# Performance work log

Measured on AMD Instinct MI355X. Metric: run time of the kernel, lower is better.

Reference implementation:

```python
import jax, jax.numpy as jnp
import numpy as np

DIM = 1024
HEADS = 16
HEAD_DIM = DIM // HEADS


def apply_rope(x):
    # x: (B, S, H, D)
    B, S, H, D = x.shape
    half = D // 2
    freqs = 1.0 / (10000.0 ** (jnp.arange(half, dtype=jnp.float32) / half))
    pos = jnp.arange(S, dtype=jnp.float32)
    angles = pos[:, None] * freqs[None, :]          # (S, half)
    sin = jnp.sin(angles)[None, :, None, :]
    cos = jnp.cos(angles)[None, :, None, :]
    x1, x2 = x[..., :half], x[..., half:]
    return jnp.concatenate([x1 * cos - x2 * sin, x1 * sin + x2 * cos], axis=-1)


def setup_inputs() -> dict:
    key = jax.random.key(0)
    ks = jax.random.split(key, 5)
    x = jax.random.normal(ks[0], (2, 2048, DIM), dtype=jnp.float32)
    s = 1.0 / np.sqrt(DIM)
    qkv_w = jax.random.uniform(ks[1], (3 * DIM, DIM), minval=-s, maxval=s, dtype=jnp.float32)
    qkv_b = jax.random.uniform(ks[2], (3 * DIM,), minval=-s, maxval=s, dtype=jnp.float32)
    proj_w = jax.random.uniform(ks[3], (DIM, DIM), minval=-s, maxval=s, dtype=jnp.float32)
    proj_b = jax.random.uniform(ks[4], (DIM,), minval=-s, maxval=s, dtype=jnp.float32)
    return {"x": x, "qkv_w": qkv_w, "qkv_b": qkv_b, "proj_w": proj_w, "proj_b": proj_b}


def reference(x, qkv_w, qkv_b, proj_w, proj_b):
    B, S, D = x.shape
    qkv = x @ qkv_w.T + qkv_b                       # (B, S, 3D)
    q, k, v = jnp.split(qkv, 3, axis=-1)
    q = q.reshape(B, S, HEADS, HEAD_DIM)
    k = k.reshape(B, S, HEADS, HEAD_DIM)
    v = v.reshape(B, S, HEADS, HEAD_DIM)
    q = apply_rope(q)
    k = apply_rope(k)
    scale = 1.0 / np.sqrt(HEAD_DIM)
    attn = jnp.einsum('bqhd,bkhd->bhqk', q, k) * scale
    mask = jnp.triu(jnp.ones((S, S), dtype=bool), k=1)
    attn = jnp.where(mask[None, None], -1e9, attn)
    attn = jax.nn.softmax(attn, axis=-1)
    out = jnp.einsum('bhqk,bkhd->bqhd', attn, v).reshape(B, S, D)
    return out @ proj_w.T + proj_b
```

## Files before the change

### kernel.cpp

```cpp
#include <hip/hip_runtime.h>
#include <hip/hip_bf16.h>
#include <stdint.h>

typedef unsigned short u16;
typedef __attribute__((ext_vector_type(8))) short bf16x8;
typedef __attribute__((ext_vector_type(4))) float f32x4;
typedef __attribute__((ext_vector_type(16))) float f32x16;

typedef __attribute__((address_space(1))) const void gas_t;
typedef __attribute__((address_space(3))) void las_t;

#define DEV __device__ __forceinline__

DEV float bf2f(u16 v){ union{uint32_t u; float f;} x; x.u = ((uint32_t)v)<<16; return x.f; }
DEV u16 f2bf(float f){ union{float f; uint32_t u;} x; x.f=f; uint32_t r = x.u + 0x7fff + ((x.u>>16)&1u); return (u16)(r>>16); }

DEV uint32_t pk2(float a, float b){
  return (uint32_t)f2bf(a) | ((uint32_t)f2bf(b)<<16);
}

DEV uint32_t cvtpk(float a, float b){
  uint32_t r;
  asm("v_cvt_pk_bf16_f32 %0, %1, %2" : "=v"(r) : "v"(a), "v"(b));
  return r;
}

DEV void xswap(uint32_t a, uint32_t b, int hi, uint32_t& ra, uint32_t& rb){
#if __has_builtin(__builtin_amdgcn_permlane32_swap)
  auto r = __builtin_amdgcn_permlane32_swap((int)a, (int)b, false, false);
  ra = (uint32_t)r[0]; rb = (uint32_t)r[1];
#else
  uint32_t sa = (uint32_t)__shfl_xor((int)a, 32);
  uint32_t sb = (uint32_t)__shfl_xor((int)b, 32);
  ra = hi ? sb : a;
  rb = hi ? b  : sa;
#endif
}

DEV void gload_lds16(const u16* g, u16* l){
  __builtin_amdgcn_global_load_lds((gas_t*)g, (las_t*)l, 16, 0, 0);
}

__global__ void cvt_f32_bf16(const float* __restrict__ src, u16* __restrict__ dst, int n4){
  int i = blockIdx.x*blockDim.x + threadIdx.x;
  if(i < n4){
    float4 v = ((const float4*)src)[i];
    ushort4 o; o.x=f2bf(v.x); o.y=f2bf(v.y); o.z=f2bf(v.z); o.w=f2bf(v.w);
    ((ushort4*)dst)[i] = o;
  }
}

template<int OUT_F32, int SWZ>
__global__ __launch_bounds__(256,3)
void gemm_bt(const u16* __restrict__ A, const u16* __restrict__ Bw,
             const float* __restrict__ bias, void* __restrict__ Cp, int N)
{
  constexpr int BK = 32, KSTEPS = 1024/BK;
  __shared__ __align__(16) u16 pool[3*8192];
  const int tid = threadIdx.x, w = tid>>6, l = tid&63;
  const int a = l&15, g = l>>4;
  int bx, by;
  if(SWZ){
    const int bid = blockIdx.x;
    const int st = bid >> 6, q = bid & 63;
    bx = (st % 3)*8 + (q & 7);
    by = (st / 3)*8 + (q >> 3);
  } else {
    bx = blockIdx.x; by = blockIdx.y;
  }
  const int m0 = by*128, n0 = bx*128;
  const int wr = w>>1, wc = w&1;
  f32x4 zero = {0.f,0.f,0.f,0.f};
  f32x4 acc[4][4];
  #pragma unroll
  for(int m=0;m<4;m++) for(int n=0;n<4;n++) acc[m][n]=zero;

  const int srow = l>>2, scol = (l&3)*8;
  const u16* Ag = A  + (size_t)(m0 + w*32 + srow)*1024 + scol;
  const u16* Bg = Bw + (size_t)(n0 + w*32 + srow)*1024 + scol;

#define STAGE(KIDX, BUF) {                                        \
    u16* ab = pool + (BUF)*8192 + w*1024;                         \
    u16* bb = pool + (BUF)*8192 + 4096 + w*1024;                  \
    gload_lds16(Ag + (KIDX)*BK,           ab);                    \
    gload_lds16(Ag + (KIDX)*BK + 16*1024, ab + 512);              \
    gload_lds16(Bg + (KIDX)*BK,           bb);                    \
    gload_lds16(Bg + (KIDX)*BK + 16*1024, bb + 512);              \
  }

  STAGE(0, 0);
  STAGE(1, 1);

  int bc = 0, bn = 2;
  for(int kt=0; kt<KSTEPS; ++kt){
    if(kt+1 < KSTEPS) asm volatile("s_waitcnt vmcnt(4)" ::: "memory");
    else              asm volatile("s_waitcnt vmcnt(0)" ::: "memory");
    __builtin_amdgcn_s_barrier();
    __builtin_amdgcn_sched_barrier(0);

    if(kt+2 < KSTEPS) STAGE(kt+2, bn);

    const u16* AsB = pool + bc*8192;
    const u16* BsB = AsB + 4096;
    bf16x8 af[4], bf[4];
    #pragma unroll
    for(int m=0;m<4;m++) af[m] = *(const bf16x8*)(AsB + (wr*64 + m*16 + a)*BK + g*8);
    #pragma unroll
    for(int n=0;n<4;n++) bf[n] = *(const bf16x8*)(BsB + (wc*64 + n*16 + a)*BK + g*8);
    #pragma unroll
    for(int m=0;m<4;m++)
      #pragma unroll
      for(int n=0;n<4;n++)
        acc[m][n] = __builtin_amdgcn_mfma_f32_16x16x32_bf16(af[m], bf[n], acc[m][n], 0,0,0);

    bc = (bc==2) ? 0 : bc+1;
    bn = (bn==2) ? 0 : bn+1;
  }
#undef STAGE

  if(OUT_F32){
    #pragma unroll
    for(int n=0;n<4;n++){
      int col = n0 + wc*64 + n*16 + a;
      float bv = bias[col];
      #pragma unroll
      for(int m=0;m<4;m++){
        int row = m0 + wr*64 + m*16 + g*4;
        #pragma unroll
        for(int r=0;r<4;r++)
          ((float*)Cp)[(size_t)(row+r)*N + col] = acc[m][n][r] + bv;
      }
    }
  } else {
    __syncthreads();
    u16* cw = pool + (size_t)w*4608;
    #pragma unroll
    for(int n=0;n<4;n++){
      float bv = bias[n0 + wc*64 + n*16 + a];
      #pragma unroll
      for(int m=0;m<4;m++)
        #pragma unroll
        for(int r=0;r<4;r++)
          cw[(m*16 + g*4 + r)*72 + n*16 + a] = f2bf(acc[m][n][r] + bv);
    }
    u16* Cb = (u16*)Cp + (size_t)(m0 + wr*64)*N + n0 + wc*64;
    #pragma unroll
    for(int rr=0;rr<8;rr++){
      int row = rr*8 + (l>>3);
      uint4 v = *(const uint4*)(cw + row*72 + (l&7)*8);
      *(uint4*)(Cb + (size_t)row*N + (l&7)*8) = v;
    }
  }
}

__global__ __launch_bounds__(256,2)
void rope_vt(const u16* __restrict__ qkv, u16* __restrict__ q_r,
             u16* __restrict__ k_r, u16* __restrict__ vt)
{
  __shared__ uint32_t L[64*65];
  const int tid = threadIdx.x;
  const int bh = blockIdx.x & 31;
  const int stile = blockIdx.x >> 5;
  const int b = bh >> 4, h = bh & 15;
  const int s0 = stile*128;

  const int cg = tid & 7, sr = tid >> 3;
  const u16* vsrc = qkv + (size_t)(b*2048 + s0)*3072 + 2048 + h*64 + cg*8;
  union U4 { uint4 v; u16 e[8]; };
  U4 v0a, v1a, v0b, v1b;
  v0a.v = *(const uint4*)(vsrc + (size_t)(sr*2    )*3072);
  v1a.v = *(const uint4*)(vsrc + (size_t)(sr*2 + 1)*3072);
  v0b.v = *(const uint4*)(vsrc + (size_t)(64 + sr*2    )*3072);
  v1b.v = *(const uint4*)(vsrc + (size_t)(64 + sr*2 + 1)*3072);
  #pragma unroll
  for(int jj=0;jj<8;jj++){
    L[(cg*8+jj)*65 + sr]      = (uint32_t)v0a.e[jj] | ((uint32_t)v1a.e[jj]<<16);
    L[(cg*8+jj)*65 + 32 + sr] = (uint32_t)v0b.e[jj] | ((uint32_t)v1b.e[jj]<<16);
  }
  __syncthreads();
  {
    const int w = tid>>6, ln = tid&63;
    u16* dst = vt + (size_t)bh*64*2048 + s0;
    #pragma unroll
    for(int dd=0;dd<16;dd++){
      int d = w*16 + dd;
      *(uint32_t*)(dst + (size_t)d*2048 + ln*2) = L[d*65 + ln];
    }
  }

  const float QSC = 0.18033688011112042f;
  #pragma unroll
  for(int it=0; it<2; ++it){
    int t2 = it*256 + tid;
    int row = t2>>2, gI = t2&3;
    int s = s0 + row;
    int d0 = gI*8;
    const u16* base = qkv + (size_t)(b*2048 + s)*3072 + h*64 + d0;
    union U { uint4 v; u16 e[8]; };
    U q1,q2,k1,k2, oq1,oq2,ok1,ok2;
    q1.v = *(const uint4*)(base);
    q2.v = *(const uint4*)(base+32);
    k1.v = *(const uint4*)(base+1024);
    k2.v = *(const uint4*)(base+1024+32);
    #pragma unroll
    for(int j=0;j<8;j++){
      float d = (float)(d0+j);
      float fr = __expf(-0.28782313662425574f * d);
      float ang = (float)s * fr;
      float sn, cs; sincosf(ang, &sn, &cs);
      float snq = sn*QSC, csq = cs*QSC;
      float x1 = bf2f(q1.e[j]), x2 = bf2f(q2.e[j]);
      oq1.e[j] = f2bf(x1*csq - x2*snq); oq2.e[j] = f2bf(x1*snq + x2*csq);
      x1 = bf2f(k1.e[j]); x2 = bf2f(k2.e[j]);
      ok1.e[j] = f2bf(x1*cs - x2*sn); ok2.e[j] = f2bf(x1*sn + x2*cs);
    }
    size_t o = ((size_t)bh*2048 + s)*64 + d0;
    *(uint4*)(q_r+o) = oq1.v; *(uint4*)(q_r+o+32) = oq2.v;
    *(uint4*)(k_r+o) = ok1.v; *(uint4*)(k_r+o+32) = ok2.v;
  }
}

__global__ __launch_bounds__(256,4)
void attn_fwd8(const u16* __restrict__ Q, const u16* __restrict__ K,
               const u16* __restrict__ VT, u16* __restrict__ O)
{
  __shared__ __align__(16) u16 Ks[2][64][64];
  __shared__ __align__(16) u16 Vs[2][64][64];
  const int tid = threadIdx.x, w = tid>>6, ln = tid&63;
  const int lo = ln&31, hi = ln>>5;
  const int wq = w>>1, wk = w&1;
  const int b0 = blockIdx.x;
  const int bh = b0 & 31;
  const int j64 = 31 - (b0 >> 5);
  const int q0 = j64*64 + wq*32;
  const int nt = j64 + 1;

  const u16* Qb = Q  + ((size_t)bh*2048 + q0)*64;
  const u16* Kb = K  + (size_t)bh*2048*64;
  const u16* Vt = VT + (size_t)bh*64*2048;

  bf16x8 qf[4];
  #pragma unroll
  for(int s=0;s<4;s++) qf[s] = *(const bf16x8*)(Qb + lo*64 + s*16 + hi*8);

  const int rsub = ln>>3;
  const int coloff = ((ln&7) ^ rsub) * 8;
  const int wrow = (w&1)*32;
  const size_t rstride = (w<2) ? 64 : 2048;
  const u16* src0 = (w<2) ? (Kb + (size_t)(wrow+rsub)*64 + coloff)
                          : (Vt + (size_t)(wrow+rsub)*2048 + coloff);
  u16* ldsw = (w<2) ? (&Ks[0][0][0] + wrow*64) : (&Vs[0][0][0] + wrow*64);

  f32x16 oacc0, oacc1, z16;
  #pragma unroll
  for(int r=0;r<16;r++){ oacc0[r]=0.f; oacc1[r]=0.f; z16[r]=0.f; }
  float l_loc = 0.f;
  const int swz = (lo&7)<<4;

  #pragma unroll
  for(int g=0;g<4;g++) gload_lds16(src0 + (size_t)g*8*rstride, ldsw + g*512);
  __syncthreads();

  int buf = 0;
  for(int t=0; t<nt; ++t){
    if(t+1 < nt){
      const size_t koff = (w<2) ? (size_t)(t+1)*64*64 : (size_t)(t+1)*64;
      u16* dst = ldsw + (buf^1)*4096;
      #pragma unroll
      for(int g=0;g<4;g++) gload_lds16(src0 + koff + (size_t)g*8*rstride, dst + g*512);
    }

    const int kv32 = t*64 + wk*32;
    if(kv32 <= q0 + 31){
      const u16* KsB = &Ks[buf][0][0];
      const u16* VsB = &Vs[buf][0][0];
      bf16x8 kf[4], vf[4];
      #pragma unroll
      for(int s=0;s<4;s++)
        kf[s] = *(const bf16x8*)(KsB + (wk*32+lo)*64 + (((s*32 + hi*16) ^ swz)>>1));
      #pragma unroll
      for(int dt=0;dt<2;dt++)
        #pragma unroll
        for(int s2=0;s2<2;s2++)
          vf[dt*2+s2] = *(const bf16x8*)(VsB + (dt*32+lo)*64 + (((wk*64 + s2*32 + hi*16) ^ swz)>>1));

      f32x16 st = __builtin_amdgcn_mfma_f32_32x32x16_bf16(kf[0], qf[0], z16, 0,0,0);
      #pragma unroll
      for(int s=1;s<4;s++)
        st = __builtin_amdgcn_mfma_f32_32x32x16_bf16(kf[s], qf[s], st, 0,0,0);

      float p[16];
      #pragma unroll
      for(int r=0;r<16;r++) p[r] = exp2f(st[r]);
      if(kv32 == q0){
        #pragma unroll
        for(int r=0;r<16;r++){
          const int kvg = (r&3) + 8*(r>>2) + 4*hi;
          p[r] = (kvg <= lo) ? p[r] : 0.f;
        }
      }

      float sm[8];
      #pragma unroll
      for(int i=0;i<8;i++) sm[i] = p[i] + p[i+8];
      #pragma unroll
      for(int s=4;s>=1;s>>=1)
        #pragma unroll
        for(int i=0;i<s;i++) sm[i] += sm[i+s];
      l_loc += sm[0];

      uint32_t pk[8];
      #pragma unroll
      for(int i=0;i<8;i++) pk[i] = cvtpk(p[2*i], p[2*i+1]);

      union PF { bf16x8 v; uint32_t u[4]; } pf0, pf1;
      xswap(pk[0], pk[2], hi, pf0.u[0], pf0.u[2]);
      xswap(pk[1], pk[3], hi, pf0.u[1], pf0.u[3]);
      xswap(pk[4], pk[6], hi, pf1.u[0], pf1.u[2]);
      xswap(pk[5], pk[7], hi, pf1.u[1], pf1.u[3]);

      oacc0 = __builtin_amdgcn_mfma_f32_32x32x16_bf16(vf[0], pf0.v, oacc0, 0,0,0);
      oacc0 = __builtin_amdgcn_mfma_f32_32x32x16_bf16(vf[1], pf1.v, oacc0, 0,0,0);
      oacc1 = __builtin_amdgcn_mfma_f32_32x32x16_bf16(vf[2], pf0.v, oacc1, 0,0,0);
      oacc1 = __builtin_amdgcn_mfma_f32_32x32x16_bf16(vf[3], pf1.v, oacc1, 0,0,0);
    }
    __syncthreads();
    buf ^= 1;
  }

  float l_run = l_loc + __shfl_xor(l_loc, 32);

  float* LoC = (float*)&Ks[0][0][0];
  float* LlC = (float*)&Vs[0][0][0];
  if(wk == 1){
    #pragma unroll
    for(int r=0;r<16;r++){
      const int d = 4*hi + (r&3) + 8*(r>>2);
      LoC[(wq*64 + d   )*32 + lo] = oacc0[r];
      LoC[(wq*64 + d+32)*32 + lo] = oacc1[r];
    }
    if(hi==0) LlC[wq*32 + lo] = l_run;
  }
  __syncthreads();
  if(wk == 0){
    l_run += LlC[wq*32 + lo];
    #pragma unroll
    for(int r=0;r<16;r++){
      const int d = 4*hi + (r&3) + 8*(r>>2);
      oacc0[r] += LoC[(wq*64 + d   )*32 + lo];
      oacc1[r] += LoC[(wq*64 + d+32)*32 + lo];
    }
    const float invl = 1.f / l_run;
    const int row_g = (bh>>4)*2048 + q0 + lo;
    u16* Ob = O + (size_t)row_g*1024 + (bh&15)*64;
    #pragma unroll
    for(int g2=0; g2<4; g2++){
      uint2 pr;
      pr.x = pk2(oacc0[4*g2+0]*invl, oacc0[4*g2+1]*invl);
      pr.y = pk2(oacc0[4*g2+2]*invl, oacc0[4*g2+3]*invl);
      *(uint2*)(Ob + 8*g2 + 4*hi) = pr;
    }
    #pragma unroll
    for(int g2=0; g2<4; g2++){
      uint2 pr;
      pr.x = pk2(oacc1[4*g2+0]*invl, oacc1[4*g2+1]*invl);
      pr.y = pk2(oacc1[4*g2+2]*invl, oacc1[4*g2+3]*invl);
      *(uint2*)(Ob + 32 + 8*g2 + 4*hi) = pr;
    }
  }
}

extern "C" void kernel_launch(void* const* d_in, const int* in_sizes, int n_in,
                              void* d_out, int out_size, void* d_ws, size_t ws_size,
                              hipStream_t stream)
{
  const float* x      = (const float*)d_in[0];
  const float* qkv_w  = (const float*)d_in[1];
  const float* qkv_b  = (const float*)d_in[2];
  const float* proj_w = (const float*)d_in[3];
  const float* proj_b = (const float*)d_in[4];
  float* out = (float*)d_out;
  char* ws = (char*)d_ws;

  u16* xb    = (u16*)(ws);
  u16* wqkv  = (u16*)(ws + 8388608);
  u16* wproj = (u16*)(ws + 8388608 + 6291456);
  u16* qkvr  = (u16*)(ws + 16777216);
  u16* q_r   = (u16*)(ws + 41943040);
  u16* k_r   = q_r + 4194304;
  u16* vt    = k_r + 4194304;
  u16* o_b   = xb;

  cvt_f32_bf16<<<4096,256,0,stream>>>(x, xb, 1048576);
  cvt_f32_bf16<<<3072,256,0,stream>>>(qkv_w, wqkv, 786432);
  cvt_f32_bf16<<<1024,256,0,stream>>>(proj_w, wproj, 262144);

  gemm_bt<0,1><<<768,256,0,stream>>>(xb, wqkv, qkv_b, qkvr, 3072);

  rope_vt<<<512,256,0,stream>>>(qkvr, q_r, k_r, vt);

  attn_fwd8<<<1024,256,0,stream>>>(q_r, k_r, vt, o_b);

  dim3 gC(8,32);
  gemm_bt<1,0><<<gC,256,0,stream>>>(o_b, wproj, proj_b, out, 1024);
}
```

Measured before the change: 109.8 us.

## Fuse RoPE and V transpose into QKV GEMM epilogue; row sums via MFMA

The QKV GEMM epilogue now applies bias, RoPE and the query scale in registers, and writes Q/K in head-major layout and V transposed straight from LDS. This removes the separate rope_vt kernel and the round trip of the intermediate qkv buffer through global memory. The attention kernel also computes the softmax row sums with an extra MFMA against a ones vector instead of a VALU reduction plus cross-lane shuffle. The cost is more sincos work per GEMM thread and two extra MFMAs per tile in attention.

```diff
diff --git a/kernel.cpp b/kernel.cpp
--- a/kernel.cpp
+++ b/kernel.cpp
@@ -50,24 +50,19 @@
   }
 }
 
-template<int OUT_F32, int SWZ>
 __global__ __launch_bounds__(256,3)
-void gemm_bt(const u16* __restrict__ A, const u16* __restrict__ Bw,
-             const float* __restrict__ bias, void* __restrict__ Cp, int N)
+void gemm_qkv(const u16* __restrict__ A, const u16* __restrict__ Bw,
+              const float* __restrict__ bias, u16* __restrict__ q_r,
+              u16* __restrict__ k_r, u16* __restrict__ vt)
 {
   constexpr int BK = 32, KSTEPS = 1024/BK;
   __shared__ __align__(16) u16 pool[3*8192];
   const int tid = threadIdx.x, w = tid>>6, l = tid&63;
   const int a = l&15, g = l>>4;
-  int bx, by;
-  if(SWZ){
-    const int bid = blockIdx.x;
-    const int st = bid >> 6, q = bid & 63;
-    bx = (st % 3)*8 + (q & 7);
-    by = (st / 3)*8 + (q >> 3);
-  } else {
-    bx = blockIdx.x; by = blockIdx.y;
-  }
+  const int bid = blockIdx.x;
+  const int st = bid >> 6, q = bid & 63;
+  const int bx = (st % 3)*8 + (q & 7);
+  const int by = (st / 3)*8 + (q >> 3);
   const int m0 = by*128, n0 = bx*128;
   const int wr = w>>1, wc = w&1;
   f32x4 zero = {0.f,0.f,0.f,0.f};
@@ -118,105 +113,129 @@
   }
 #undef STAGE
 
-  if(OUT_F32){
+  __syncthreads();
+  u16* cw = pool + (size_t)w*4608;
+  const int kind = bx >> 3;
+  const int h = (bx&7)*2 + wc;
+  const int bh = (by>>4)*16 + h;
+  const int s_base = (by&15)*128 + wr*64;
+
+  if(kind < 2){
+    const float QSC = kind==0 ? 0.18033688011112042f : 1.0f;
+    #pragma unroll
+    for(int n=0;n<2;n++){
+      const float fr = __expf(-0.28782313662425574f * (float)(n*16+a));
+      const float b1 = bias[bx*128 + wc*64 + n*16 + a];
+      const float b2 = bias[bx*128 + wc*64 + n*16 + a + 32];
+      #pragma unroll
+      for(int m=0;m<4;m++)
+        #pragma unroll
+        for(int r=0;r<4;r++){
+          const int sr2 = m*16 + g*4 + r;
+          float sn, cs; sincosf((float)(s_base + sr2) * fr, &sn, &cs);
+          sn *= QSC; cs *= QSC;
+          const float x1 = acc[m][n][r] + b1;
+          const float x2 = acc[m][n+2][r] + b2;
+          cw[sr2*72 + n*16 + a]      = f2bf(x1*cs - x2*sn);
+          cw[sr2*72 + n*16 + a + 32] = f2bf(x1*sn + x2*cs);
+        }
+    }
+    u16* Ob = (kind==0 ? q_r : k_r) + ((size_t)bh*2048 + s_base)*64;
+    #pragma unroll
+    for(int rr=0;rr<8;rr++){
+      const int row = rr*8 + (l>>3);
+      uint4 v = *(const uint4*)(cw + row*72 + (l&7)*8);
+      *(uint4*)(Ob + (size_t)row*64 + (l&7)*8) = v;
+    }
+  } else {
     #pragma unroll
     for(int n=0;n<4;n++){
-      int col = n0 + wc*64 + n*16 + a;
-      float bv = bias[col];
-      #pragma unroll
-      for(int m=0;m<4;m++){
-        int row = m0 + wr*64 + m*16 + g*4;
-        #pragma unroll
-        for(int r=0;r<4;r++)
-          ((float*)Cp)[(size_t)(row+r)*N + col] = acc[m][n][r] + bv;
-      }
-    }
-  } else {
-    __syncthreads();
-    u16* cw = pool + (size_t)w*4608;
-    #pragma unroll
-    for(int n=0;n<4;n++){
-      float bv = bias[n0 + wc*64 + n*16 + a];
+      const float bv = bias[bx*128 + wc*64 + n*16 + a];
       #pragma unroll
       for(int m=0;m<4;m++)
         #pragma unroll
         for(int r=0;r<4;r++)
-          cw[(m*16 + g*4 + r)*72 + n*16 + a] = f2bf(acc[m][n][r] + bv);
-    }
-    u16* Cb = (u16*)Cp + (size_t)(m0 + wr*64)*N + n0 + wc*64;
+          cw[(n*16+a)*72 + m*16 + g*4 + r] = f2bf(acc[m][n][r] + bv);
+    }
+    u16* Ob = vt + (size_t)bh*64*2048 + s_base;
     #pragma unroll
     for(int rr=0;rr<8;rr++){
-      int row = rr*8 + (l>>3);
-      uint4 v = *(const uint4*)(cw + row*72 + (l&7)*8);
-      *(uint4*)(Cb + (size_t)row*N + (l&7)*8) = v;
-    }
-  }
-}
-
-__global__ __launch_bounds__(256,2)
-void rope_vt(const u16* __restrict__ qkv, u16* __restrict__ q_r,
-             u16* __restrict__ k_r, u16* __restrict__ vt)
+      const int d = rr*8 + (l>>3);
+      uint4 v = *(const uint4*)(cw + d*72 + (l&7)*8);
+      *(uint4*)(Ob + (size_t)d*2048 + (l&7)*8) = v;
+    }
+  }
+}
+
+__global__ __launch_bounds__(256,3)
+void gemm_proj(const u16* __restrict__ A, const u16* __restrict__ Bw,
+               const float* __restrict__ bias, float* __restrict__ Cp, int N)
 {
-  __shared__ uint32_t L[64*65];
-  const int tid = threadIdx.x;
-  const int bh = blockIdx.x & 31;
-  const int stile = blockIdx.x >> 5;
-  const int b = bh >> 4, h = bh & 15;
-  const int s0 = stile*128;
-
-  const int cg = tid & 7, sr = tid >> 3;
-  const u16* vsrc = qkv + (size_t)(b*2048 + s0)*3072 + 2048 + h*64 + cg*8;
-  union U4 { uint4 v; u16 e[8]; };
-  U4 v0a, v1a, v0b, v1b;
-  v0a.v = *(const uint4*)(vsrc + (size_t)(sr*2    )*3072);
-  v1a.v = *(const uint4*)(vsrc + (size_t)(sr*2 + 1)*3072);
-  v0b.v = *(const uint4*)(vsrc + (size_t)(64 + sr*2    )*3072);
-  v1b.v = *(const uint4*)(vsrc + (size_t)(64 + sr*2 + 1)*3072);
-  #pragma unroll
-  for(int jj=0;jj<8;jj++){
-    L[(cg*8+jj)*65 + sr]      = (uint32_t)v0a.e[jj] | ((uint32_t)v1a.e[jj]<<16);
-    L[(cg*8+jj)*65 + 32 + sr] = (uint32_t)v0b.e[jj] | ((uint32_t)v1b.e[jj]<<16);
-  }
-  __syncthreads();
-  {
-    const int w = tid>>6, ln = tid&63;
-    u16* dst = vt + (size_t)bh*64*2048 + s0;
-    #pragma unroll
-    for(int dd=0;dd<16;dd++){
-      int d = w*16 + dd;
-      *(uint32_t*)(dst + (size_t)d*2048 + ln*2) = L[d*65 + ln];
-    }
-  }
-
-  const float QSC = 0.18033688011112042f;
-  #pragma unroll
-  for(int it=0; it<2; ++it){
-    int t2 = it*256 + tid;
-    int row = t2>>2, gI = t2&3;
-    int s = s0 + row;
-    int d0 = gI*8;
-    const u16* base = qkv + (size_t)(b*2048 + s)*3072 + h*64 + d0;
-    union U { uint4 v; u16 e[8]; };
-    U q1,q2,k1,k2, oq1,oq2,ok1,ok2;
-    q1.v = *(const uint4*)(base);
-    q2.v = *(const uint4*)(base+32);
-    k1.v = *(const uint4*)(base+1024);
-    k2.v = *(const uint4*)(base+1024+32);
-    #pragma unroll
-    for(int j=0;j<8;j++){
-      float d = (float)(d0+j);
-      float fr = __expf(-0.28782313662425574f * d);
-      float ang = (float)s * fr;
-      float sn, cs; sincosf(ang, &sn, &cs);
-      float snq = sn*QSC, csq = cs*QSC;
-      float x1 = bf2f(q1.e[j]), x2 = bf2f(q2.e[j]);
-      oq1.e[j] = f2bf(x1*csq - x2*snq); oq2.e[j] = f2bf(x1*snq + x2*csq);
-      x1 = bf2f(k1.e[j]); x2 = bf2f(k2.e[j]);
-      ok1.e[j] = f2bf(x1*cs - x2*sn); ok2.e[j] = f2bf(x1*sn + x2*cs);
-    }
-    size_t o = ((size_t)bh*2048 + s)*64 + d0;
-    *(uint4*)(q_r+o) = oq1.v; *(uint4*)(q_r+o+32) = oq2.v;
-    *(uint4*)(k_r+o) = ok1.v; *(uint4*)(k_r+o+32) = ok2.v;
+  constexpr int BK = 32, KSTEPS = 1024/BK;
+  __shared__ __align__(16) u16 pool[3*8192];
+  const int tid = threadIdx.x, w = tid>>6, l = tid&63;
+  const int a = l&15, g = l>>4;
+  const int m0 = blockIdx.y*128, n0 = blockIdx.x*128;
+  const int wr = w>>1, wc = w&1;
+  f32x4 zero = {0.f,0.f,0.f,0.f};
+  f32x4 acc[4][4];
+  #pragma unroll
+  for(int m=0;m<4;m++) for(int n=0;n<4;n++) acc[m][n]=zero;
+
+  const int srow = l>>2, scol = (l&3)*8;
+  const u16* Ag = A  + (size_t)(m0 + w*32 + srow)*1024 + scol;
+  const u16* Bg = Bw + (size_t)(n0 + w*32 + srow)*1024 + scol;
+
+#define STAGE(KIDX, BUF) {                                        \
+    u16* ab = pool + (BUF)*8192 + w*1024;                         \
+    u16* bb = pool + (BUF)*8192 + 4096 + w*1024;                  \
+    gload_lds16(Ag + (KIDX)*BK,           ab);                    \
+    gload_lds16(Ag + (KIDX)*BK + 16*1024, ab + 512);              \
+    gload_lds16(Bg + (KIDX)*BK,           bb);                    \
+    gload_lds16(Bg + (KIDX)*BK + 16*1024, bb + 512);              \
+  }
+
+  STAGE(0, 0);
+  STAGE(1, 1);
+
+  int bc = 0, bn = 2;
+  for(int kt=0; kt<KSTEPS; ++kt){
+    if(kt+1 < KSTEPS) asm volatile("s_waitcnt vmcnt(4)" ::: "memory");
+    else              asm volatile("s_waitcnt vmcnt(0)" ::: "memory");
+    __builtin_amdgcn_s_barrier();
+    __builtin_amdgcn_sched_barrier(0);
+
+    if(kt+2 < KSTEPS) STAGE(kt+2, bn);
+
+    const u16* AsB = pool + bc*8192;
+    const u16* BsB = AsB + 4096;
+    bf16x8 af[4], bf[4];
+    #pragma unroll
+    for(int m=0;m<4;m++) af[m] = *(const bf16x8*)(AsB + (wr*64 + m*16 + a)*BK + g*8);
+    #pragma unroll
+    for(int n=0;n<4;n++) bf[n] = *(const bf16x8*)(BsB + (wc*64 + n*16 + a)*BK + g*8);
+    #pragma unroll
+    for(int m=0;m<4;m++)
+      #pragma unroll
+      for(int n=0;n<4;n++)
+        acc[m][n] = __builtin_amdgcn_mfma_f32_16x16x32_bf16(af[m], bf[n], acc[m][n], 0,0,0);
+
+    bc = (bc==2) ? 0 : bc+1;
+    bn = (bn==2) ? 0 : bn+1;
+  }
+#undef STAGE
+
+  #pragma unroll
+  for(int n=0;n<4;n++){
+    int col = n0 + wc*64 + n*16 + a;
+    float bv = bias[col];
+    #pragma unroll
+    for(int m=0;m<4;m++){
+      int row = m0 + wr*64 + m*16 + g*4;
+      #pragma unroll
+      for(int r=0;r<4;r++)
+        Cp[(size_t)(row+r)*N + col] = acc[m][n][r] + bv;
+    }
   }
 }
 
@@ -251,10 +270,12 @@
                           : (Vt + (size_t)(wrow+rsub)*2048 + coloff);
   u16* ldsw = (w<2) ? (&Ks[0][0][0] + wrow*64) : (&Vs[0][0][0] + wrow*64);
 
-  f32x16 oacc0, oacc1, z16;
-  #pragma unroll
-  for(int r=0;r<16;r++){ oacc0[r]=0.f; oacc1[r]=0.f; z16[r]=0.f; }
-  float l_loc = 0.f;
+  f32x16 oacc0, oacc1, lacc, z16;
+  #pragma unroll
+  for(int r=0;r<16;r++){ oacc0[r]=0.f; oacc1[r]=0.f; lacc[r]=0.f; z16[r]=0.f; }
+  bf16x8 vones;
+  #pragma unroll
+  for(int i=0;i<8;i++) vones[i] = (short)0x3F80;
   const int swz = (lo&7)<<4;
 
   #pragma unroll
@@ -300,15 +321,6 @@
         }
       }
 
-      float sm[8];
-      #pragma unroll
-      for(int i=0;i<8;i++) sm[i] = p[i] + p[i+8];
-      #pragma unroll
-      for(int s=4;s>=1;s>>=1)
-        #pragma unroll
-        for(int i=0;i<s;i++) sm[i] += sm[i+s];
-      l_loc += sm[0];
-
       uint32_t pk[8];
       #pragma unroll
       for(int i=0;i<8;i++) pk[i] = cvtpk(p[2*i], p[2*i+1]);
@@ -323,12 +335,14 @@
       oacc0 = __builtin_amdgcn_mfma_f32_32x32x16_bf16(vf[1], pf1.v, oacc0, 0,0,0);
       oacc1 = __builtin_amdgcn_mfma_f32_32x32x16_bf16(vf[2], pf0.v, oacc1, 0,0,0);
       oacc1 = __builtin_amdgcn_mfma_f32_32x32x16_bf16(vf[3], pf1.v, oacc1, 0,0,0);
+      lacc  = __builtin_amdgcn_mfma_f32_32x32x16_bf16(vones, pf0.v, lacc, 0,0,0);
+      lacc  = __builtin_amdgcn_mfma_f32_32x32x16_bf16(vones, pf1.v, lacc, 0,0,0);
     }
     __syncthreads();
     buf ^= 1;
   }
 
-  float l_run = l_loc + __shfl_xor(l_loc, 32);
+  float l_run = lacc[0];
 
   float* LoC = (float*)&Ks[0][0][0];
   float* LlC = (float*)&Vs[0][0][0];
@@ -385,8 +399,7 @@
   u16* xb    = (u16*)(ws);
   u16* wqkv  = (u16*)(ws + 8388608);
   u16* wproj = (u16*)(ws + 8388608 + 6291456);
-  u16* qkvr  = (u16*)(ws + 16777216);
-  u16* q_r   = (u16*)(ws + 41943040);
+  u16* q_r   = (u16*)(ws + 16777216);
   u16* k_r   = q_r + 4194304;
   u16* vt    = k_r + 4194304;
   u16* o_b   = xb;
@@ -395,12 +408,10 @@
   cvt_f32_bf16<<<3072,256,0,stream>>>(qkv_w, wqkv, 786432);
   cvt_f32_bf16<<<1024,256,0,stream>>>(proj_w, wproj, 262144);
 
-  gemm_bt<0,1><<<768,256,0,stream>>>(xb, wqkv, qkv_b, qkvr, 3072);
-
-  rope_vt<<<512,256,0,stream>>>(qkvr, q_r, k_r, vt);
+  gemm_qkv<<<768,256,0,stream>>>(xb, wqkv, qkv_b, q_r, k_r, vt);
 
   attn_fwd8<<<1024,256,0,stream>>>(q_r, k_r, vt, o_b);
 
   dim3 gC(8,32);
-  gemm_bt<1,0><<<gC,256,0,stream>>>(o_b, wproj, proj_b, out, 1024);
-}
+  gemm_proj<<<gC,256,0,stream>>>(o_b, wproj, proj_b, out, 1024);
+}
```

New measurement: 122.8 us. 11.8% more time.
